# Kernel tuning notes

Measured on AMD Instinct MI355X. Metric: run time of the kernel, lower is better.

Reference implementation:

```python
import jax, jax.numpy as jnp
import numpy as np

B, N, S = 8, 8192, 2048
IN, SKIP, OUT, EXP = 256, 128, 256, 4
GROUPS = 8


def conv1d(x, w, b):
    # 1x1 conv: x [B,C,N], w [O,C], b [O]
    return jnp.einsum('bcn,oc->bon', x, w) + b[None, :, None]


def group_norm(x, w, b, groups=GROUPS, eps=1e-5):
    Bb, C, Nn = x.shape
    xg = x.reshape(Bb, groups, C // groups, Nn)
    m = xg.mean(axis=(2, 3), keepdims=True)
    v = xg.var(axis=(2, 3), keepdims=True)
    xn = ((xg - m) * jax.lax.rsqrt(v + eps)).reshape(Bb, C, Nn)
    return xn * w[None, :, None] + b[None, :, None]


def _forward(xyz1, points1, xyz2, points2, t_emb, c_emb,
             mlp_w, mlp_b, mlp_gw, mlp_gb,
             c1w, c1b, g1w, g1b, c2w, c2b, g2w, g2b,
             tw, tb, cw, cb):
    # pairwise squared distances [B,N,S]
    dists = (-2.0 * jnp.einsum('bcn,bcm->bnm', xyz1, xyz2)
             + jnp.sum(xyz1 ** 2, axis=1)[:, :, None]
             + jnp.sum(xyz2 ** 2, axis=1)[:, None, :])
    neg_d3, idx = jax.lax.top_k(-dists, 3)          # 3 smallest distances
    d3 = -neg_d3                                     # [B,N,3]
    recip = 1.0 / (d3 + 1e-8)
    weight = recip / jnp.sum(recip, axis=2, keepdims=True)
    # gather neighbor features: points2 [B,C,S], idx [B,N,3] -> [B,C,N,3]
    gathered = jax.vmap(lambda p, i: p[:, i])(points2, idx)
    interp = jnp.sum(gathered * weight[:, None, :, :], axis=3)  # [B,IN,N]

    new_points = jnp.concatenate([points1, interp], axis=1)     # [B,IN+SKIP,N]
    x = jax.nn.silu(group_norm(conv1d(new_points, mlp_w, mlp_b), mlp_gw, mlp_gb))

    identity = x
    h = jax.nn.silu(group_norm(conv1d(x, c1w, c1b), g1w, g1b))
    h = group_norm(conv1d(h, c2w, c2b), g2w, g2b)
    st = t_emb @ tw.T + tb
    sc = c_emb @ cw.T + cb
    scale_t, shift_t = jnp.split(st, 2, axis=1)
    scale_c, shift_c = jnp.split(sc, 2, axis=1)
    scale = (scale_t + scale_c)[:, :, None]
    shift = (shift_t + shift_c)[:, :, None]
    h = h * (1.0 + scale) + shift
    return h + identity


def setup_inputs() -> dict:
    key = jax.random.key(0)
    ks = jax.random.split(key, 12)
    def rn(k, shape, s=1.0):
        return jax.random.normal(k, shape, dtype=jnp.float32) * s
    E = OUT * EXP
    return dict(
        xyz1=rn(ks[0], (B, 3, N)),
        points1=rn(ks[1], (B, SKIP, N)),
        xyz2=rn(ks[2], (B, 3, S)),
        points2=rn(ks[3], (B, IN, S)),
        t_emb=rn(ks[4], (B, OUT)),
        c_emb=rn(ks[5], (B, OUT)),
        mlp_w=rn(ks[6], (OUT, IN + SKIP), 0.02), mlp_b=jnp.zeros((OUT,), jnp.float32),
        mlp_gw=jnp.ones((OUT,), jnp.float32), mlp_gb=jnp.zeros((OUT,), jnp.float32),
        c1w=rn(ks[7], (E, OUT), 0.02), c1b=jnp.zeros((E,), jnp.float32),
        g1w=jnp.ones((E,), jnp.float32), g1b=jnp.zeros((E,), jnp.float32),
        c2w=rn(ks[8], (OUT, E), 0.02), c2b=jnp.zeros((OUT,), jnp.float32),
        g2w=jnp.ones((OUT,), jnp.float32), g2b=jnp.zeros((OUT,), jnp.float32),
        tw=rn(ks[9], (2 * OUT, OUT), 0.02), tb=jnp.zeros((2 * OUT,), jnp.float32),
        cw=rn(ks[10], (2 * OUT, OUT), 0.02), cb=jnp.zeros((2 * OUT,), jnp.float32),
    )


def reference(xyz1, points1, xyz2, points2, t_emb, c_emb,
              mlp_w, mlp_b, mlp_gw, mlp_gb,
              c1w, c1b, g1w, g1b, c2w, c2b, g2w, g2b,
              tw, tb, cw, cb):
    return _forward(xyz1, points1, xyz2, points2, t_emb, c_emb,
                    mlp_w, mlp_b, mlp_gw, mlp_gb,
                    c1w, c1b, g1w, g1b, c2w, c2b, g2w, g2b,
                    tw, tb, cw, cb)
```

## Files before the change

kernel.cpp:

```cpp
#include <hip/hip_runtime.h>
#include <hip/hip_bf16.h>

typedef unsigned short u16;
typedef __attribute__((ext_vector_type(4))) float f32x4;
typedef __attribute__((ext_vector_type(8))) short bf16x8;

typedef const __attribute__((address_space(1))) void GV;
typedef __attribute__((address_space(3))) void LV;
#define GLOAD16(g, l) __builtin_amdgcn_global_load_lds((GV*)(g), (LV*)(l), 16, 0, 0)

__device__ __forceinline__ float b2f(u16 u) {
    union { float f; unsigned int i; } v; v.i = ((unsigned int)u) << 16; return v.f;
}
__device__ __forceinline__ u16 f2b(float f) {
    union { float f; unsigned int i; } v; v.f = f;
    unsigned int x = v.i;
    return (u16)((x + 0x7fffu + ((x >> 16) & 1u)) >> 16);
}
__device__ __forceinline__ unsigned int cvt_pk_bf16(float lo, float hi) {
    unsigned int d;
    asm("v_cvt_pk_bf16_f32 %0, %1, %2" : "=v"(d) : "v"(lo), "v"(hi));
    return d;
}
__device__ __forceinline__ float silu(float t) {
    return t * __builtin_amdgcn_rcpf(1.f + __expf(-t));
}

__global__ void knn_part_kernel(const float* __restrict__ xyz1, const float* __restrict__ xyz2,
                                float2* __restrict__ cand) {
    __shared__ float4 spt[256];
    int b = blockIdx.z, ck = blockIdx.y, tid = threadIdx.x;
    const float* p2 = xyz2 + (size_t)b * 3 * 2048;
    int s0 = ck << 8;
    {
        int s = s0 + tid;
        float x = p2[s], y = p2[2048 + s], z = p2[4096 + s];
        spt[tid] = make_float4(x, y, z, (x * x + y * y) + z * z);
    }
    __syncthreads();
    int n = blockIdx.x * 256 + tid;
    const float* p1 = xyz1 + (size_t)b * 3 * 8192;
    float qx = p1[n], qy = p1[8192 + n], qz = p1[16384 + n];
    float qn = (qx * qx + qy * qy) + qz * qz;
    float d0 = 3.4e38f, d1 = 3.4e38f, d2 = 3.4e38f;
    int i0 = 0, i1 = 0, i2 = 0;
#pragma unroll 4
    for (int s = 0; s < 256; ++s) {
        float4 p = spt[s];
        float dot = (qx * p.x + qy * p.y) + qz * p.z;
        float d = (-2.f * dot + qn) + p.w;
        if (d < d2) {
            int gi = s0 + s;
            if (d < d1) {
                if (d < d0) { d2 = d1; i2 = i1; d1 = d0; i1 = i0; d0 = d; i0 = gi; }
                else        { d2 = d1; i2 = i1; d1 = d;  i1 = gi; }
            } else          { d2 = d;  i2 = gi; }
        }
    }
    float2* c = cand + (((size_t)b * 8192 + n) * 8 + ck) * 3;
    c[0] = make_float2(d0, __int_as_float(i0));
    c[1] = make_float2(d1, __int_as_float(i1));
    c[2] = make_float2(d2, __int_as_float(i2));
}

__global__ void knn_merge_kernel(const float2* __restrict__ cand,
                                 int* __restrict__ idx_out, float* __restrict__ w_out) {
    int t = blockIdx.x * 256 + threadIdx.x;
    const float2* c = cand + (size_t)t * 24;
    float d0 = 3.4e38f, d1 = 3.4e38f, d2 = 3.4e38f;
    int i0 = 0, i1 = 0, i2 = 0;
#pragma unroll
    for (int k = 0; k < 24; ++k) {
        float2 p = c[k];
        float d = p.x;
        if (d < d2) {
            int gi = __float_as_int(p.y);
            if (d < d1) {
                if (d < d0) { d2 = d1; i2 = i1; d1 = d0; i1 = i0; d0 = d; i0 = gi; }
                else        { d2 = d1; i2 = i1; d1 = d;  i1 = gi; }
            } else          { d2 = d;  i2 = gi; }
        }
    }
    float r0 = 1.f / (d0 + 1e-8f), r1 = 1.f / (d1 + 1e-8f), r2 = 1.f / (d2 + 1e-8f);
    float inv = 1.f / (r0 + r1 + r2);
    size_t base = (size_t)t * 3;
    idx_out[base] = i0; idx_out[base + 1] = i1; idx_out[base + 2] = i2;
    w_out[base] = r0 * inv; w_out[base + 1] = r1 * inv; w_out[base + 2] = r2 * inv;
}

__global__ void tr_kernel(const float* __restrict__ src, u16* __restrict__ dst, int C, int S) {
    __shared__ u16 tile[64][70];
    int b = blockIdx.z;
    int s0 = blockIdx.x * 64, c0 = blockIdx.y * 64;
    int tid = threadIdx.x, lane = tid & 63, wv = tid >> 6;
    const float* sp = src + ((size_t)b * C + c0) * S + s0;
    for (int c = wv; c < 64; c += 4)
        tile[lane][c] = f2b(sp[(size_t)c * S + lane]);
    __syncthreads();
    u16* dp = dst + ((size_t)b * S + s0) * C + c0;
    int s = tid >> 5, cp = tid & 31;
#pragma unroll
    for (int k = 0; k < 8; ++k) {
        int r = s + k * 8;
        unsigned int v = *(const unsigned int*)&tile[r][cp * 2];
        *(unsigned int*)&dp[(size_t)r * C + cp * 2] = v;
    }
}

__global__ void build_x0_kernel(const u16* __restrict__ p1t, const u16* __restrict__ p2t,
                                const int* __restrict__ idx, const float* __restrict__ wgt,
                                u16* __restrict__ x0t) {
    int b = blockIdx.y;
    int n = blockIdx.x * 64 + (threadIdx.x >> 2);
    int q = threadIdx.x & 3;
    size_t ib = ((size_t)b * 8192 + n) * 3;
    int j0 = idx[ib], j1 = idx[ib + 1], j2 = idx[ib + 2];
    float w0 = wgt[ib], w1 = wgt[ib + 1], w2 = wgt[ib + 2];
    const u16* pr = p1t + ((size_t)b * 8192 + n) * 128;
    const u16* r0 = p2t + ((size_t)b * 2048 + j0) * 256;
    const u16* r1 = p2t + ((size_t)b * 2048 + j1) * 256;
    const u16* r2 = p2t + ((size_t)b * 2048 + j2) * 256;
    u16* out = x0t + ((size_t)b * 8192 + n) * 384;
#pragma unroll
    for (int i = 0; i < 4; ++i) {
        int ch = (i * 4 + q) * 8;
        *(uint4*)&out[ch] = *(const uint4*)&pr[ch];
    }
#pragma unroll
    for (int i = 0; i < 8; ++i) {
        int c = (i * 4 + q) * 8;
        bf16x8 a0 = *(const bf16x8*)&r0[c];
        bf16x8 a1 = *(const bf16x8*)&r1[c];
        bf16x8 a2 = *(const bf16x8*)&r2[c];
        u16 ovu[8] __attribute__((aligned(16)));
#pragma unroll
        for (int j = 0; j < 8; ++j) {
            float v = w0 * b2f((u16)a0[j]) + w1 * b2f((u16)a1[j]) + w2 * b2f((u16)a2[j]);
            ovu[j] = f2b(v);
        }
        *(uint4*)&out[128 + c] = *(const uint4*)ovu;
    }
}

__global__ void cvt_kernel(const float* __restrict__ src, u16* __restrict__ dst, int n) {
    int i = blockIdx.x * 256 + threadIdx.x;
    if (i < n) dst[i] = f2b(src[i]);
}

__global__ void film_kernel(const float* __restrict__ t_emb, const float* __restrict__ c_emb,
                            const float* __restrict__ tw, const float* __restrict__ tb,
                            const float* __restrict__ cw, const float* __restrict__ cb,
                            float* __restrict__ film) {
    __shared__ float te[256], ce[256];
    int b = blockIdx.x, tid = threadIdx.x;
    te[tid] = t_emb[b * 256 + tid];
    ce[tid] = c_emb[b * 256 + tid];
    __syncthreads();
    int j = tid + blockIdx.y * 256;
    const float* twr = tw + (size_t)j * 256;
    const float* cwr = cw + (size_t)j * 256;
    float s = 0.f;
    for (int k = 0; k < 256; ++k) s += te[k] * twr[k] + ce[k] * cwr[k];
    s += tb[j] + cb[j];
    film[b * 512 + j] = s;
}

__global__ __launch_bounds__(512, 4) void gemm_kernel(
        const u16* __restrict__ At, const u16* __restrict__ W, const float* __restrict__ bias,
        u16* __restrict__ Out, float* __restrict__ part,
        int K, int M, int gshift) {
    __shared__ u16 lA[2][128 * 64];
    __shared__ u16 lB[2][128 * 64];
    __shared__ float bpart[4][2];
    int b = blockIdx.z;
    int n0 = blockIdx.x * 128, o0 = blockIdx.y * 128;
    int tid = threadIdx.x, lane = tid & 63, wv = tid >> 6;
    int wn = wv & 1, wo = wv >> 1;
    if (tid < 8) ((float*)bpart)[tid] = 0.f;
    f32x4 acc[4][2];
#pragma unroll
    for (int i = 0; i < 4; i++)
#pragma unroll
        for (int j = 0; j < 2; j++) acc[i][j] = (f32x4){0.f, 0.f, 0.f, 0.f};

    int rl = lane >> 3;
    int csw = ((lane & 7) ^ rl) * 8;
    const u16* aP[2];
    const u16* bP[2];
#pragma unroll
    for (int p2 = 0; p2 < 2; p2++) {
        int p = wv * 2 + p2;
        aP[p2] = At + ((size_t)b * 8192 + n0 + p * 8 + rl) * K + csw;
        bP[p2] = W + ((size_t)(o0 + p * 8 + rl)) * K + csw;
    }
    int nK = K >> 6;
#pragma unroll
    for (int p2 = 0; p2 < 2; p2++) {
        int p = wv * 2 + p2;
        GLOAD16(aP[p2], &lA[0][p * 512]);
        GLOAD16(bP[p2], &lB[0][p * 512]);
        aP[p2] += 64; bP[p2] += 64;
    }
    asm volatile("s_waitcnt vmcnt(0) lgkmcnt(0)" ::: "memory");
    __builtin_amdgcn_s_barrier();
    int cur = 0;
    for (int kt = 0; kt < nK; ++kt) {
        if (kt + 1 < nK) {
#pragma unroll
            for (int p2 = 0; p2 < 2; p2++) {
                int p = wv * 2 + p2;
                GLOAD16(aP[p2], &lA[cur ^ 1][p * 512]);
                GLOAD16(bP[p2], &lB[cur ^ 1][p * 512]);
                aP[p2] += 64; bP[p2] += 64;
            }
        }
        const u16* la = lA[cur];
        const u16* lb = lB[cur];
#pragma unroll
        for (int kk = 0; kk < 2; kk++) {
            bf16x8 af[4], bfr[2];
#pragma unroll
            for (int mf = 0; mf < 4; mf++) {
                int R = wn * 64 + mf * 16 + (lane & 15);
                af[mf] = *(const bf16x8*)&la[R * 64 + ((kk * 4 + (lane >> 4)) ^ (R & 7)) * 8];
            }
#pragma unroll
            for (int nf = 0; nf < 2; nf++) {
                int R = wo * 32 + nf * 16 + (lane & 15);
                bfr[nf] = *(const bf16x8*)&lb[R * 64 + ((kk * 4 + (lane >> 4)) ^ (R & 7)) * 8];
            }
#pragma unroll
            for (int mf = 0; mf < 4; mf++)
#pragma unroll
                for (int nf = 0; nf < 2; nf++)
                    acc[mf][nf] = __builtin_amdgcn_mfma_f32_16x16x32_bf16(bfr[nf], af[mf], acc[mf][nf], 0, 0, 0);
        }
        if (kt + 1 < nK)
            asm volatile("s_waitcnt vmcnt(0)" ::: "memory");
        __builtin_amdgcn_s_barrier();
        cur ^= 1;
    }
    int oq = (lane >> 4) * 4;
    float4 bs[2];
    float s1[2] = {0.f, 0.f}, s2[2] = {0.f, 0.f};
#pragma unroll
    for (int nf = 0; nf < 2; nf++) bs[nf] = *(const float4*)&bias[o0 + wo * 32 + nf * 16 + oq];
#pragma unroll
    for (int mf = 0; mf < 4; mf++) {
        int n = n0 + wn * 64 + mf * 16 + (lane & 15);
        u16* rowp = Out + ((size_t)b * 8192 + n) * M + o0 + wo * 32 + oq;
#pragma unroll
        for (int nf = 0; nf < 2; nf++) {
            float v0 = acc[mf][nf][0] + bs[nf].x;
            float v1 = acc[mf][nf][1] + bs[nf].y;
            float v2 = acc[mf][nf][2] + bs[nf].z;
            float v3 = acc[mf][nf][3] + bs[nf].w;
            s1[nf] += (v0 + v1) + (v2 + v3);
            s2[nf] += (v0 * v0 + v1 * v1) + (v2 * v2 + v3 * v3);
            uint2 pk;
            pk.x = cvt_pk_bf16(v0, v1);
            pk.y = cvt_pk_bf16(v2, v3);
            *(uint2*)&rowp[nf * 16] = pk;
        }
    }
#pragma unroll
    for (int nf = 0; nf < 2; nf++) {
        float a = s1[nf], c = s2[nf];
#pragma unroll
        for (int off = 32; off > 0; off >>= 1) {
            a += __shfl_xor(a, off, 64);
            c += __shfl_xor(c, off, 64);
        }
        if (lane == 0) {
            int gl = (wo * 32 + nf * 16) >> gshift;
            atomicAdd(&bpart[gl][0], a);
            atomicAdd(&bpart[gl][1], c);
        }
    }
    __syncthreads();
    int nlg = 128 >> gshift;
    if (tid < 2 * nlg) {
        int gl = tid >> 1, s = tid & 1;
        int g = (o0 >> gshift) + gl;
        part[(((size_t)b * 8 + g) * 2 + s) * 64 + blockIdx.x] = bpart[gl][s];
    }
}

__global__ __launch_bounds__(512, 4) void gemm_gn_kernel(
        const u16* __restrict__ At, const u16* __restrict__ W, const float* __restrict__ bias,
        const float* __restrict__ tab,
        u16* __restrict__ Out, float* __restrict__ part,
        int K, int M, int gshift) {
    __shared__ u16 lA[2][128 * 64];
    __shared__ u16 lB[2][128 * 64];
    __shared__ float cA[1024], cB[1024];
    __shared__ float bpart[4][2];
    int b = blockIdx.z;
    int n0 = blockIdx.x * 128, o0 = blockIdx.y * 128;
    int tid = threadIdx.x, lane = tid & 63, wv = tid >> 6;
    int wn = wv & 1, wo = wv >> 1;
    if (tid < 8) ((float*)bpart)[tid] = 0.f;
    f32x4 acc[4][2];
#pragma unroll
    for (int i = 0; i < 4; i++)
#pragma unroll
        for (int j = 0; j < 2; j++) acc[i][j] = (f32x4){0.f, 0.f, 0.f, 0.f};

    int rl = lane >> 3;
    int csw = ((lane & 7) ^ rl) * 8;
    const u16* aP[2];
    const u16* bP[2];
#pragma unroll
    for (int p2 = 0; p2 < 2; p2++) {
        int p = wv * 2 + p2;
        aP[p2] = At + ((size_t)b * 8192 + n0 + p * 8 + rl) * K + csw;
        bP[p2] = W + ((size_t)(o0 + p * 8 + rl)) * K + csw;
    }
    int nK = K >> 6;
    uint4 areg[2];
#pragma unroll
    for (int p2 = 0; p2 < 2; p2++) { areg[p2] = *(const uint4*)aP[p2]; aP[p2] += 64; }
#pragma unroll
    for (int p2 = 0; p2 < 2; p2++) {
        int p = wv * 2 + p2;
        GLOAD16(bP[p2], &lB[0][p * 512]);
        bP[p2] += 64;
    }
    {
        const float* tA = tab + (size_t)b * K;
        const float* tB = tab + (size_t)(8 + b) * K;
        for (int i = tid; i < K; i += 512) { cA[i] = tA[i]; cB[i] = tB[i]; }
    }
    __syncthreads();
#pragma unroll
    for (int p2 = 0; p2 < 2; p2++) {
        int p = wv * 2 + p2;
        int c = csw;
        const u16* rr = (const u16*)&areg[p2];
        float4 a0 = *(const float4*)&cA[c], a1 = *(const float4*)&cA[c + 4];
        float4 b0 = *(const float4*)&cB[c], b1 = *(const float4*)&cB[c + 4];
        float va[8] = {a0.x, a0.y, a0.z, a0.w, a1.x, a1.y, a1.z, a1.w};
        float vb[8] = {b0.x, b0.y, b0.z, b0.w, b1.x, b1.y, b1.z, b1.w};
        float v[8];
#pragma unroll
        for (int j = 0; j < 8; ++j) v[j] = silu(b2f(rr[j]) * va[j] + vb[j]);
        uint4 o;
        o.x = cvt_pk_bf16(v[0], v[1]); o.y = cvt_pk_bf16(v[2], v[3]);
        o.z = cvt_pk_bf16(v[4], v[5]); o.w = cvt_pk_bf16(v[6], v[7]);
        *(uint4*)&lA[0][p * 512 + lane * 8] = o;
    }
    asm volatile("s_waitcnt vmcnt(0) lgkmcnt(0)" ::: "memory");
    __builtin_amdgcn_s_barrier();
    int cur = 0;
    for (int kt = 0; kt < nK; ++kt) {
        if (kt + 1 < nK) {
#pragma unroll
            for (int p2 = 0; p2 < 2; p2++) { areg[p2] = *(const uint4*)aP[p2]; aP[p2] += 64; }
#pragma unroll
            for (int p2 = 0; p2 < 2; p2++) {
                int p = wv * 2 + p2;
                GLOAD16(bP[p2], &lB[cur ^ 1][p * 512]);
                bP[p2] += 64;
            }
        }
        const u16* la = lA[cur];
        const u16* lb = lB[cur];
#pragma unroll
        for (int kk = 0; kk < 2; kk++) {
            bf16x8 af[4], bfr[2];
#pragma unroll
            for (int mf = 0; mf < 4; mf++) {
                int R = wn * 64 + mf * 16 + (lane & 15);
                af[mf] = *(const bf16x8*)&la[R * 64 + ((kk * 4 + (lane >> 4)) ^ (R & 7)) * 8];
            }
#pragma unroll
            for (int nf = 0; nf < 2; nf++) {
                int R = wo * 32 + nf * 16 + (lane & 15);
                bfr[nf] = *(const bf16x8*)&lb[R * 64 + ((kk * 4 + (lane >> 4)) ^ (R & 7)) * 8];
            }
#pragma unroll
            for (int mf = 0; mf < 4; mf++)
#pragma unroll
                for (int nf = 0; nf < 2; nf++)
                    acc[mf][nf] = __builtin_amdgcn_mfma_f32_16x16x32_bf16(bfr[nf], af[mf], acc[mf][nf], 0, 0, 0);
        }
        if (kt + 1 < nK) {
            int c = (kt + 1) * 64 + csw;
            float4 a0 = *(const float4*)&cA[c], a1 = *(const float4*)&cA[c + 4];
            float4 b0 = *(const float4*)&cB[c], b1 = *(const float4*)&cB[c + 4];
            float va[8] = {a0.x, a0.y, a0.z, a0.w, a1.x, a1.y, a1.z, a1.w};
            float vb[8] = {b0.x, b0.y, b0.z, b0.w, b1.x, b1.y, b1.z, b1.w};
#pragma unroll
            for (int p2 = 0; p2 < 2; p2++) {
                int p = wv * 2 + p2;
                const u16* rr = (const u16*)&areg[p2];
                float v[8];
#pragma unroll
                for (int j = 0; j < 8; ++j) v[j] = silu(b2f(rr[j]) * va[j] + vb[j]);
                uint4 o;
                o.x = cvt_pk_bf16(v[0], v[1]); o.y = cvt_pk_bf16(v[2], v[3]);
                o.z = cvt_pk_bf16(v[4], v[5]); o.w = cvt_pk_bf16(v[6], v[7]);
                *(uint4*)&lA[cur ^ 1][p * 512 + lane * 8] = o;
            }
            asm volatile("s_waitcnt vmcnt(0)" ::: "memory");
        }
        asm volatile("s_waitcnt lgkmcnt(0)" ::: "memory");
        __builtin_amdgcn_s_barrier();
        cur ^= 1;
    }
    int oq = (lane >> 4) * 4;
    float4 bs[2];
    float s1[2] = {0.f, 0.f}, s2[2] = {0.f, 0.f};
#pragma unroll
    for (int nf = 0; nf < 2; nf++) bs[nf] = *(const float4*)&bias[o0 + wo * 32 + nf * 16 + oq];
#pragma unroll
    for (int mf = 0; mf < 4; mf++) {
        int n = n0 + wn * 64 + mf * 16 + (lane & 15);
        u16* rowp = Out + ((size_t)b * 8192 + n) * M + o0 + wo * 32 + oq;
#pragma unroll
        for (int nf = 0; nf < 2; nf++) {
            float v0 = acc[mf][nf][0] + bs[nf].x;
            float v1 = acc[mf][nf][1] + bs[nf].y;
            float v2 = acc[mf][nf][2] + bs[nf].z;
            float v3 = acc[mf][nf][3] + bs[nf].w;
            s1[nf] += (v0 + v1) + (v2 + v3);
            s2[nf] += (v0 * v0 + v1 * v1) + (v2 * v2 + v3 * v3);
            uint2 pk;
            pk.x = cvt_pk_bf16(v0, v1);
            pk.y = cvt_pk_bf16(v2, v3);
            *(uint2*)&rowp[nf * 16] = pk;
        }
    }
#pragma unroll
    for (int nf = 0; nf < 2; nf++) {
        float a = s1[nf], c = s2[nf];
#pragma unroll
        for (int off = 32; off > 0; off >>= 1) {
            a += __shfl_xor(a, off, 64);
            c += __shfl_xor(c, off, 64);
        }
        if (lane == 0) {
            int gl = (wo * 32 + nf * 16) >> gshift;
            atomicAdd(&bpart[gl][0], a);
            atomicAdd(&bpart[gl][1], c);
        }
    }
    __syncthreads();
    int nlg = 128 >> gshift;
    if (tid < 2 * nlg) {
        int gl = tid >> 1, s = tid & 1;
        int g = (o0 >> gshift) + gl;
        part[(((size_t)b * 8 + g) * 2 + s) * 64 + blockIdx.x] = bpart[gl][s];
    }
}

__global__ void gn_reduce_kernel(const float* __restrict__ part, float* __restrict__ stats) {
    int t = threadIdx.x;
    const float4* p = (const float4*)(part + (size_t)t * 64);
    float s = 0.f;
#pragma unroll
    for (int i = 0; i < 16; i++) { float4 v = p[i]; s += (v.x + v.y) + (v.z + v.w); }
    stats[t] = s;
}

__global__ void gn_coef_kernel(const float* __restrict__ stats, const float* __restrict__ gw,
                               const float* __restrict__ gb, float* __restrict__ tab,
                               int K, int gshift, float invCnt) {
    int c = blockIdx.x * 256 + threadIdx.x;
    int b = blockIdx.y;
    int g = c >> gshift;
    float sum = stats[(b * 8 + g) * 2], ssq = stats[(b * 8 + g) * 2 + 1];
    float m = sum * invCnt;
    float rstd = rsqrtf(fmaxf(ssq * invCnt - m * m, 0.f) + 1e-5f);
    float A = rstd * gw[c];
    tab[(size_t)b * K + c] = A;
    tab[(size_t)(8 + b) * K + c] = gb[c] - m * A;
}

__global__ void final_kernel(const u16* __restrict__ Y2, const u16* __restrict__ Xraw,
                             const float* __restrict__ g0w, const float* __restrict__ g0b,
                             const float* __restrict__ stats0,
                             const float* __restrict__ g2w, const float* __restrict__ g2b,
                             const float* __restrict__ stats2, const float* __restrict__ film,
                             float* __restrict__ out) {
    __shared__ float tile[64][257];
    int b = blockIdx.y, n0 = blockIdx.x * 64, tid = threadIdx.x;
    const float invCnt = 1.f / (32.f * 8192.f);
    int c8 = tid & 31, c0 = c8 << 3, g = c8 >> 2;
    float sum = stats2[(b * 8 + g) * 2], ssq = stats2[(b * 8 + g) * 2 + 1];
    float m = sum * invCnt, rstd = rsqrtf(fmaxf(ssq * invCnt - m * m, 0.f) + 1e-5f);
    float sum0 = stats0[(b * 8 + g) * 2], ssq0 = stats0[(b * 8 + g) * 2 + 1];
    float m0 = sum0 * invCnt, rstd0 = rsqrtf(fmaxf(ssq0 * invCnt - m0 * m0, 0.f) + 1e-5f);
    float4 w0 = *(const float4*)(g2w + c0), w1 = *(const float4*)(g2w + c0 + 4);
    float4 q0 = *(const float4*)(g2b + c0), q1 = *(const float4*)(g2b + c0 + 4);
    float4 f0 = *(const float4*)(film + b * 512 + c0), f1 = *(const float4*)(film + b * 512 + c0 + 4);
    float4 h0 = *(const float4*)(film + b * 512 + 256 + c0), h1 = *(const float4*)(film + b * 512 + 256 + c0 + 4);
    float4 u0 = *(const float4*)(g0w + c0), u1 = *(const float4*)(g0w + c0 + 4);
    float4 e0 = *(const float4*)(g0b + c0), e1 = *(const float4*)(g0b + c0 + 4);
    float wv[8] = {w0.x, w0.y, w0.z, w0.w, w1.x, w1.y, w1.z, w1.w};
    float qv[8] = {q0.x, q0.y, q0.z, q0.w, q1.x, q1.y, q1.z, q1.w};
    float fs[8] = {f0.x, f0.y, f0.z, f0.w, f1.x, f1.y, f1.z, f1.w};
    float fh[8] = {h0.x, h0.y, h0.z, h0.w, h1.x, h1.y, h1.z, h1.w};
    float uv[8] = {u0.x, u0.y, u0.z, u0.w, u1.x, u1.y, u1.z, u1.w};
    float ev[8] = {e0.x, e0.y, e0.z, e0.w, e1.x, e1.y, e1.z, e1.w};
    float A[8], Bc[8], A0[8], B0[8];
#pragma unroll
    for (int j = 0; j < 8; j++) {
        float sc = 1.f + fs[j];
        A[j] = rstd * wv[j] * sc;
        Bc[j] = (qv[j] - m * rstd * wv[j]) * sc + fh[j];
        A0[j] = rstd0 * uv[j];
        B0[j] = ev[j] - m0 * A0[j];
    }
    int nrb = tid >> 5;
#pragma unroll
    for (int k = 0; k < 8; k++) {
        int nr = nrb + k * 8;
        size_t base = ((size_t)b * 8192 + n0 + nr) * 256 + c0;
        uint4 yv = *(const uint4*)(Y2 + base);
        uint4 xv = *(const uint4*)(Xraw + base);
        const u16* yy = (const u16*)&yv;
        const u16* xx = (const u16*)&xv;
#pragma unroll
        for (int j = 0; j < 8; j++) {
            float x = silu(b2f(xx[j]) * A0[j] + B0[j]);
            tile[nr][c0 + j] = b2f(yy[j]) * A[j] + Bc[j] + x;
        }
    }
    __syncthreads();
    for (int q = tid; q < 256 * 16; q += 256) {
        int c = q >> 4, n4 = q & 15;
        float4 o;
        o.x = tile[n4 * 4 + 0][c];
        o.y = tile[n4 * 4 + 1][c];
        o.z = tile[n4 * 4 + 2][c];
        o.w = tile[n4 * 4 + 3][c];
        *(float4*)&out[((size_t)b * 256 + c) * 8192 + n0 + n4 * 4] = o;
    }
}

extern "C" void kernel_launch(void* const* d_in, const int* in_sizes, int n_in,
                              void* d_out, int out_size, void* d_ws, size_t ws_size,
                              hipStream_t stream) {
    const float* xyz1    = (const float*)d_in[0];
    const float* points1 = (const float*)d_in[1];
    const float* xyz2    = (const float*)d_in[2];
    const float* points2 = (const float*)d_in[3];
    const float* t_emb   = (const float*)d_in[4];
    const float* c_emb   = (const float*)d_in[5];
    const float* mlp_w   = (const float*)d_in[6];
    const float* mlp_b   = (const float*)d_in[7];
    const float* mlp_gw  = (const float*)d_in[8];
    const float* mlp_gb  = (const float*)d_in[9];
    const float* c1w     = (const float*)d_in[10];
    const float* c1b     = (const float*)d_in[11];
    const float* g1w     = (const float*)d_in[12];
    const float* g1b     = (const float*)d_in[13];
    const float* c2w     = (const float*)d_in[14];
    const float* c2b     = (const float*)d_in[15];
    const float* g2w     = (const float*)d_in[16];
    const float* g2b     = (const float*)d_in[17];
    const float* tw      = (const float*)d_in[18];
    const float* tb      = (const float*)d_in[19];
    const float* cw      = (const float*)d_in[20];
    const float* cb      = (const float*)d_in[21];

    char* ws = (char*)d_ws;
    int*   idx    = (int*)ws;
    float* wgt    = (float*)(ws + 786432);
    float* stats0 = (float*)(ws + 1572864);
    float* stats1 = (float*)(ws + 1573376);
    float* stats2 = (float*)(ws + 1573888);
    float* film   = (float*)(ws + 1574400);
    float* part0  = (float*)(ws + 1590784);
    float* part1  = (float*)(ws + 1623552);
    float* part2  = (float*)(ws + 1656320);
    u16* wb_mlp   = (u16*)(ws + 1689088);
    u16* wb_c1    = (u16*)(ws + 1885696);
    u16* wb_c2    = (u16*)(ws + 2409984);
    float* tab0   = (float*)(ws + 2934272);
    float* tab1   = (float*)(ws + 2950656);
    u16* X0t = (u16*)(ws + 4194304);
    u16* Y1t = (u16*)(ws + 54525952);
    u16* H1t = (u16*)(ws + 88080384);
    u16* Y2t = X0t;
    float2* cand = (float2*)X0t;
    u16* p1t = H1t;
    u16* p2t = H1t + 8388608ull;
    float* out = (float*)d_out;

    cvt_kernel<<<384, 256, 0, stream>>>(mlp_w, wb_mlp, 98304);
    cvt_kernel<<<1024, 256, 0, stream>>>(c1w, wb_c1, 262144);
    cvt_kernel<<<1024, 256, 0, stream>>>(c2w, wb_c2, 262144);
    knn_part_kernel<<<dim3(32, 8, 8), 256, 0, stream>>>(xyz1, xyz2, cand);
    knn_merge_kernel<<<256, 256, 0, stream>>>(cand, idx, wgt);
    tr_kernel<<<dim3(128, 2, 8), 256, 0, stream>>>(points1, p1t, 128, 8192);
    tr_kernel<<<dim3(32, 4, 8), 256, 0, stream>>>(points2, p2t, 256, 2048);
    build_x0_kernel<<<dim3(128, 8), 256, 0, stream>>>(p1t, p2t, idx, wgt, X0t);
    film_kernel<<<dim3(8, 2), 256, 0, stream>>>(t_emb, c_emb, tw, tb, cw, cb, film);
    gemm_kernel<<<dim3(64, 2, 8), 512, 0, stream>>>(X0t, wb_mlp, mlp_b, Y1t, part0, 384, 256, 5);
    gn_reduce_kernel<<<1, 128, 0, stream>>>(part0, stats0);
    gn_coef_kernel<<<dim3(1, 8), 256, 0, stream>>>(stats0, mlp_gw, mlp_gb, tab0, 256, 5, 1.f / (32.f * 8192.f));
    gemm_gn_kernel<<<dim3(64, 8, 8), 512, 0, stream>>>(Y1t, wb_c1, c1b, tab0, H1t, part1, 256, 1024, 7);
    gn_reduce_kernel<<<1, 128, 0, stream>>>(part1, stats1);
    gn_coef_kernel<<<dim3(4, 8), 256, 0, stream>>>(stats1, g1w, g1b, tab1, 1024, 7, 1.f / (128.f * 8192.f));
    gemm_gn_kernel<<<dim3(64, 2, 8), 512, 0, stream>>>(H1t, wb_c2, c2b, tab1, Y2t, part2, 1024, 256, 5);
    gn_reduce_kernel<<<1, 128, 0, stream>>>(part2, stats2);
    final_kernel<<<dim3(128, 8), 256, 0, stream>>>(Y2t, Y1t, mlp_gw, mlp_gb, stats0,
                                                   g2w, g2b, stats2, film, out);
}
```

Before: 374.2 us.

## Transpose points1 directly into X0 and pre-apply first GroupNorm before c1 GEMM

The points1 transpose now writes straight into the strided X0 buffer, so build_x0 no longer copies the skip channels through an intermediate. The first GroupNorm+SiLU becomes a standalone elementwise pass that writes activated Y1 once. The 1024-wide c1 GEMM can then use the plain GEMM kernel instead of the one that normalizes its input on load. Normalization is no longer repeated across the 8 output-column tiles, at the cost of an extra launch and a read/write pass over Y1.

```diff
diff --git a/kernel.cpp b/kernel.cpp
--- a/kernel.cpp
+++ b/kernel.cpp
@@ -88,7 +88,8 @@
     w_out[base] = r0 * inv; w_out[base + 1] = r1 * inv; w_out[base + 2] = r2 * inv;
 }
 
-__global__ void tr_kernel(const float* __restrict__ src, u16* __restrict__ dst, int C, int S) {
+__global__ void tr_kernel(const float* __restrict__ src, u16* __restrict__ dst,
+                          int C, int S, int dstStride) {
     __shared__ u16 tile[64][70];
     int b = blockIdx.z;
     int s0 = blockIdx.x * 64, c0 = blockIdx.y * 64;
@@ -97,17 +98,17 @@
     for (int c = wv; c < 64; c += 4)
         tile[lane][c] = f2b(sp[(size_t)c * S + lane]);
     __syncthreads();
-    u16* dp = dst + ((size_t)b * S + s0) * C + c0;
+    u16* dp = dst + ((size_t)b * S + s0) * dstStride + c0;
     int s = tid >> 5, cp = tid & 31;
 #pragma unroll
     for (int k = 0; k < 8; ++k) {
         int r = s + k * 8;
         unsigned int v = *(const unsigned int*)&tile[r][cp * 2];
-        *(unsigned int*)&dp[(size_t)r * C + cp * 2] = v;
-    }
-}
-
-__global__ void build_x0_kernel(const u16* __restrict__ p1t, const u16* __restrict__ p2t,
+        *(unsigned int*)&dp[(size_t)r * dstStride + cp * 2] = v;
+    }
+}
+
+__global__ void build_x0_kernel(const u16* __restrict__ p2t,
                                 const int* __restrict__ idx, const float* __restrict__ wgt,
                                 u16* __restrict__ x0t) {
     int b = blockIdx.y;
@@ -116,16 +117,10 @@
     size_t ib = ((size_t)b * 8192 + n) * 3;
     int j0 = idx[ib], j1 = idx[ib + 1], j2 = idx[ib + 2];
     float w0 = wgt[ib], w1 = wgt[ib + 1], w2 = wgt[ib + 2];
-    const u16* pr = p1t + ((size_t)b * 8192 + n) * 128;
     const u16* r0 = p2t + ((size_t)b * 2048 + j0) * 256;
     const u16* r1 = p2t + ((size_t)b * 2048 + j1) * 256;
     const u16* r2 = p2t + ((size_t)b * 2048 + j2) * 256;
     u16* out = x0t + ((size_t)b * 8192 + n) * 384;
-#pragma unroll
-    for (int i = 0; i < 4; ++i) {
-        int ch = (i * 4 + q) * 8;
-        *(uint4*)&out[ch] = *(const uint4*)&pr[ch];
-    }
 #pragma unroll
     for (int i = 0; i < 8; ++i) {
         int c = (i * 4 + q) * 8;
@@ -475,6 +470,38 @@
     float A = rstd * gw[c];
     tab[(size_t)b * K + c] = A;
     tab[(size_t)(8 + b) * K + c] = gb[c] - m * A;
+}
+
+__global__ void gn_apply_kernel(const u16* __restrict__ Yin, u16* __restrict__ Yout,
+                                const float* __restrict__ tab) {
+    int t = blockIdx.x * 256 + threadIdx.x;
+    int c8 = t & 31, c0 = c8 << 3;
+    int row0 = t >> 5;
+    int rowstep = (gridDim.x * 256) >> 5;
+    float A[8], Bc[8];
+    int bprev = -1;
+    for (int row = row0; row < 65536; row += rowstep) {
+        int b = row >> 13;
+        if (b != bprev) {
+            bprev = b;
+            float4 a0 = *(const float4*)(tab + (size_t)b * 256 + c0);
+            float4 a1 = *(const float4*)(tab + (size_t)b * 256 + c0 + 4);
+            float4 b0 = *(const float4*)(tab + (size_t)(8 + b) * 256 + c0);
+            float4 b1 = *(const float4*)(tab + (size_t)(8 + b) * 256 + c0 + 4);
+            A[0]=a0.x;A[1]=a0.y;A[2]=a0.z;A[3]=a0.w;A[4]=a1.x;A[5]=a1.y;A[6]=a1.z;A[7]=a1.w;
+            Bc[0]=b0.x;Bc[1]=b0.y;Bc[2]=b0.z;Bc[3]=b0.w;Bc[4]=b1.x;Bc[5]=b1.y;Bc[6]=b1.z;Bc[7]=b1.w;
+        }
+        size_t off = ((size_t)row << 8) + c0;
+        uint4 v4 = *(const uint4*)(Yin + off);
+        const u16* vu = (const u16*)&v4;
+        float v[8];
+#pragma unroll
+        for (int j = 0; j < 8; j++) v[j] = silu(b2f(vu[j]) * A[j] + Bc[j]);
+        uint4 o;
+        o.x = cvt_pk_bf16(v[0], v[1]); o.y = cvt_pk_bf16(v[2], v[3]);
+        o.z = cvt_pk_bf16(v[4], v[5]); o.w = cvt_pk_bf16(v[6], v[7]);
+        *(uint4*)(Yout + off) = o;
+    }
 }
 
 __global__ void final_kernel(const u16* __restrict__ Y2, const u16* __restrict__ Xraw,
@@ -584,9 +611,9 @@
     u16* Y1t = (u16*)(ws + 54525952);
     u16* H1t = (u16*)(ws + 88080384);
     u16* Y2t = X0t;
+    u16* Y1act = X0t;
     float2* cand = (float2*)X0t;
-    u16* p1t = H1t;
-    u16* p2t = H1t + 8388608ull;
+    u16* p2t = H1t;
     float* out = (float*)d_out;
 
     cvt_kernel<<<384, 256, 0, stream>>>(mlp_w, wb_mlp, 98304);
@@ -594,14 +621,15 @@
     cvt_kernel<<<1024, 256, 0, stream>>>(c2w, wb_c2, 262144);
     knn_part_kernel<<<dim3(32, 8, 8), 256, 0, stream>>>(xyz1, xyz2, cand);
     knn_merge_kernel<<<256, 256, 0, stream>>>(cand, idx, wgt);
-    tr_kernel<<<dim3(128, 2, 8), 256, 0, stream>>>(points1, p1t, 128, 8192);
-    tr_kernel<<<dim3(32, 4, 8), 256, 0, stream>>>(points2, p2t, 256, 2048);
-    build_x0_kernel<<<dim3(128, 8), 256, 0, stream>>>(p1t, p2t, idx, wgt, X0t);
+    tr_kernel<<<dim3(128, 2, 8), 256, 0, stream>>>(points1, X0t, 128, 8192, 384);
+    tr_kernel<<<dim3(32, 4, 8), 256, 0, stream>>>(points2, p2t, 256, 2048, 256);
+    build_x0_kernel<<<dim3(128, 8), 256, 0, stream>>>(p2t, idx, wgt, X0t);
     film_kernel<<<dim3(8, 2), 256, 0, stream>>>(t_emb, c_emb, tw, tb, cw, cb, film);
     gemm_kernel<<<dim3(64, 2, 8), 512, 0, stream>>>(X0t, wb_mlp, mlp_b, Y1t, part0, 384, 256, 5);
     gn_reduce_kernel<<<1, 128, 0, stream>>>(part0, stats0);
     gn_coef_kernel<<<dim3(1, 8), 256, 0, stream>>>(stats0, mlp_gw, mlp_gb, tab0, 256, 5, 1.f / (32.f * 8192.f));
-    gemm_gn_kernel<<<dim3(64, 8, 8), 512, 0, stream>>>(Y1t, wb_c1, c1b, tab0, H1t, part1, 256, 1024, 7);
+    gn_apply_kernel<<<512, 256, 0, stream>>>(Y1t, Y1act, tab0);
+    gemm_kernel<<<dim3(64, 8, 8), 512, 0, stream>>>(Y1act, wb_c1, c1b, H1t, part1, 256, 1024, 7);
     gn_reduce_kernel<<<1, 128, 0, stream>>>(part1, stats1);
     gn_coef_kernel<<<dim3(4, 8), 256, 0, stream>>>(stats1, g1w, g1b, tab1, 1024, 7, 1.f / (128.f * 8192.f));
     gemm_gn_kernel<<<dim3(64, 2, 8), 512, 0, stream>>>(H1t, wb_c2, c2b, tab1, Y2t, part2, 1024, 256, 5);
```

Result: faster. 360.0 us (-3.8%).
